# Kernel tuning notes

Measured on AMD Instinct MI355X. Metric: run time of the kernel, lower is better.

Reference implementation:

```python
import jax, jax.numpy as jnp
import numpy as np

D, IN_CH, H, W = 4, 13, 384, 384
EMBED, HID, N_COLORS = 64, 32, 11


def conv(x, w, b, stride=1, pad=0):
    y = jax.lax.conv_general_dilated(
        x, w, window_strides=(stride, stride),
        padding=[(pad, pad), (pad, pad)],
        dimension_numbers=('NCHW', 'OIHW', 'NCHW'))
    return y + b[None, :, None, None]


def setup_inputs() -> dict:
    key = jax.random.key(0)
    ks = jax.random.split(key, 16)
    s = 0.05
    return {
        'demo_inputs': jax.random.normal(ks[0], (D, IN_CH, H, W), jnp.float32),
        'demo_outputs': jax.random.normal(ks[1], (D, IN_CH, H, W), jnp.float32),
        'test_input': jax.random.normal(ks[2], (IN_CH, H, W), jnp.float32),
        'enc_w1': jax.random.normal(ks[3], (32, 26, 3, 3), jnp.float32) * s,
        'enc_b1': jnp.zeros((32,), jnp.float32),
        'enc_w2': jax.random.normal(ks[4], (64, 32, 3, 3), jnp.float32) * s,
        'enc_b2': jnp.zeros((64,), jnp.float32),
        'enc_w3': jax.random.normal(ks[5], (64, 64, 3, 3), jnp.float32) * s,
        'enc_b3': jnp.zeros((64,), jnp.float32),
        'enc_lw': jax.random.normal(ks[6], (EMBED, 64), jnp.float32) * s,
        'enc_lb': jnp.zeros((EMBED,), jnp.float32),
        'stem_w': jax.random.normal(ks[7], (HID, IN_CH, 3, 3), jnp.float32) * s,
        'stem_b': jnp.zeros((HID,), jnp.float32),
        'upd_w1': jax.random.normal(ks[8], (HID, HID + EMBED, 3, 3), jnp.float32) * s,
        'upd_b1': jnp.zeros((HID,), jnp.float32),
        'upd_w2': jax.random.normal(ks[9], (HID, HID, 1, 1), jnp.float32) * s,
        'upd_b2': jnp.zeros((HID,), jnp.float32),
        'tau_w': jax.random.normal(ks[10], (HID, HID + EMBED, 1, 1), jnp.float32) * s,
        'tau_b': jnp.zeros((HID,), jnp.float32),
        'dec_w': jax.random.normal(ks[11], (N_COLORS, HID, 1, 1), jnp.float32) * s,
        'dec_b': jnp.zeros((N_COLORS,), jnp.float32),
        'n_steps': 8,
    }


def reference(demo_inputs, demo_outputs, test_input,
              enc_w1, enc_b1, enc_w2, enc_b2, enc_w3, enc_b3, enc_lw, enc_lb,
              stem_w, stem_b, upd_w1, upd_b1, upd_w2, upd_b2,
              tau_w, tau_b, dec_w, dec_b, n_steps):
    # encode_demos: concat each (in, out) pair along channels -> [D, 2*in_ch, H, W]
    pairs = jnp.concatenate([demo_inputs, demo_outputs], axis=1)
    h = jax.nn.relu(conv(pairs, enc_w1, enc_b1, stride=1, pad=1))
    h = jax.nn.relu(conv(h, enc_w2, enc_b2, stride=2, pad=1))
    h = jax.nn.relu(conv(h, enc_w3, enc_b3, stride=2, pad=1))
    h = h.mean(axis=(2, 3))                      # AdaptiveAvgPool2d(1) + Flatten -> [D, 64]
    emb = h @ enc_lw.T + enc_lb                  # [D, embed_dim]
    task_embed = emb.mean(axis=0)                # [embed_dim]

    x = test_input[None]                         # [1, in_ch, H, W]
    Hh, Ww = x.shape[2], x.shape[3]
    te = jnp.broadcast_to(task_embed[None, :, None, None], (1, task_embed.shape[0], Hh, Ww))
    state = jax.nn.relu(conv(x, stem_w, stem_b, stride=1, pad=1))
    for _ in range(n_steps):
        ctx = jnp.concatenate([state, te], axis=1)   # [1, hid+embed, H, W]
        delta = conv(jax.nn.relu(conv(ctx, upd_w1, upd_b1, stride=1, pad=1)),
                     upd_w2, upd_b2, stride=1, pad=0)
        beta = jax.nn.sigmoid(conv(ctx, tau_w, tau_b, stride=1, pad=0))
        state = beta * state + (1.0 - beta) * delta
    return conv(state, dec_w, dec_b, stride=1, pad=0)  # [1, N_COLORS, H, W]
```

## Files before the change

kernel.cpp:

```cpp
#include <hip/hip_runtime.h>

#define HW 147456

typedef __attribute__((ext_vector_type(8))) short bf16x8;
typedef __attribute__((ext_vector_type(4))) float f32x4;

__device__ __forceinline__ float bf2f(unsigned short u) {
    return __uint_as_float(((unsigned)u) << 16);
}
__device__ __forceinline__ unsigned short f2bf(float f) {
    unsigned u = __float_as_uint(f);
    return (unsigned short)((u + 0x7fffu + ((u >> 16) & 1u)) >> 16);
}

struct TJobs {
    const float* src[5];
    float* dst[5];
    int cout[5], cintot[5], k[5], coutp[5];
    int start[6];
};

__global__ __launch_bounds__(256) void transpose_all_k(TJobs J) {
    int gid = blockIdx.x * 256 + threadIdx.x;
    if (gid >= J.start[5]) return;
    int j = 0;
#pragma unroll
    for (int t = 1; t < 5; ++t)
        if (gid >= J.start[t]) j = t;
    int li = gid - J.start[j];
    int coutp = J.coutp[j], K = J.k[j];
    int co = li % coutp;
    int kk = (li / coutp) % K;
    int cin = li / (coutp * K);
    J.dst[j][li] = (co < J.cout[j]) ? J.src[j][((co * J.cintot[j]) + cin) * K + kk] : 0.f;
}

struct WJobs {
    const float* src[4];
    unsigned short* dst[4];
    int cout[4], cin[4], cintot[4], cinp[4];
    int start[5];
};

__global__ __launch_bounds__(256) void transpose_wbf_k(WJobs J) {
    int gid = blockIdx.x * 256 + threadIdx.x;
    if (gid >= J.start[4]) return;
    int j = 0;
#pragma unroll
    for (int t = 1; t < 4; ++t)
        if (gid >= J.start[t]) j = t;
    int li = gid - J.start[j];
    int cinp = J.cinp[j];
    int ci = li % cinp;
    int co = (li / cinp) % J.cout[j];
    int tap = li / (cinp * J.cout[j]);
    float v = (ci < J.cin[j]) ? J.src[j][((co * J.cintot[j]) + ci) * 9 + tap] : 0.f;
    J.dst[j][li] = f2bf(v);
}

template <int CIN, int CP, int COUT, int S, int OX, int OY, int MW, bool RELU>
__global__ __launch_bounds__(256, MW) void mfma_conv_k(
    const float* __restrict__ in0, const float* __restrict__ in1, int split,
    long off0base, long off1base, long zs0, long zs1, int inW, int inH,
    const unsigned short* __restrict__ wB,
    const float* __restrict__ bias,
    float* __restrict__ out, long outZS) {
    constexpr int XT = (OX - 1) * S + 3;
    constexpr int YT = (OY - 1) * S + 3;
    constexpr int CINK = (CIN + 31) & ~31;
    constexpr int KST = CINK / 32;
    constexpr int NCG = COUT / 16;
    constexpr int NTX = OX / 16;
    constexpr int NSP = NTX * OY;
    constexpr int NTASK = NSP * NCG;
    constexpr int NT4 = NTASK / 4;
    constexpr int NSLOT = YT * XT;
    static_assert(NTASK % 4 == 0, "tasks per wave");
    static_assert(NSP % NT4 == 0, "wave must own a single cout-group");
    static_assert(CP % 8 == 0 && CP >= CINK, "LDS cin pad");
    static_assert((CP / 8) % 2 == 1, "odd chunk stride for bank spread");
    __shared__ __align__(16) unsigned short tile[NSLOT * CP];
    const int tid = threadIdx.x;
    const int bx = blockIdx.x, by = blockIdx.y, z = blockIdx.z;
    const long o0 = off0base + (long)z * zs0;
    const long o1 = off1base + (long)z * zs1;
    const int outW = inW / S, outH = inH / S;
    const int gx0 = bx * OX * S - 1;
    const int gy0 = by * OY * S - 1;

#pragma unroll 1
    for (int s = tid; s < NSLOT; s += 256) {
        const int sy = s / XT;
        const int lx = s - sy * XT;
        const int gy = gy0 + sy;
        const int gx = gx0 + lx;
        const bool ok = ((unsigned)gy < (unsigned)inH) && ((unsigned)gx < (unsigned)inW);
        const long pix = (long)gy * inW + gx;
#pragma unroll
        for (int h = 0; h < CINK / 8; ++h) {
            bf16x8 v;
#pragma unroll
            for (int e = 0; e < 8; ++e) {
                const int c = h * 8 + e;
                float f = 0.f;
                if (c < CIN && ok) {
                    const float* base = (c < split)
                        ? in0 + o0 + (long)c * inH * inW
                        : in1 + o1 + (long)(c - split) * inH * inW;
                    f = base[pix];
                }
                v[e] = (short)f2bf(f);
            }
            *(bf16x8*)(tile + s * CP + h * 8) = v;
        }
    }
    __syncthreads();

    const int wv = tid >> 6;
    const int l = tid & 63;
    const int ln = l & 15;
    const int lk = l >> 4;
    const int cg = (wv * NT4) / NSP;
    bf16x8 bfr[9 * KST];
#pragma unroll
    for (int tap = 0; tap < 9; ++tap)
#pragma unroll
        for (int h = 0; h < KST; ++h)
            bfr[tap * KST + h] = *(const bf16x8*)(wB + ((long)(tap * COUT + cg * 16 + ln)) * CINK + h * 32 + lk * 8);
    const float bv = bias[cg * 16 + ln];
#pragma unroll 1
    for (int t = 0; t < NT4; ++t) {
        const int sp = wv * NT4 + t - cg * NSP;
        const int tx = sp % NTX;
        const int ty = sp / NTX;
        f32x4 acc;
        acc[0] = bv; acc[1] = bv; acc[2] = bv; acc[3] = bv;
#pragma unroll
        for (int ky = 0; ky < 3; ++ky) {
#pragma unroll
            for (int kx = 0; kx < 3; ++kx) {
                const int yb = ty * S + ky;
                const int xb = (tx * 16 + ln) * S + kx;
                const unsigned short* ap = tile + (yb * XT + xb) * CP + lk * 8;
#pragma unroll
                for (int h = 0; h < KST; ++h) {
                    bf16x8 a = *(const bf16x8*)(ap + h * 32);
                    acc = __builtin_amdgcn_mfma_f32_16x16x32_bf16(a, bfr[(ky * 3 + kx) * KST + h], acc, 0, 0, 0);
                }
            }
        }
        const int ox = bx * OX + tx * 16 + lk * 4;
        const int oy = by * OY + ty;
        float4 o;
        if constexpr (RELU) {
            o.x = fmaxf(acc[0], 0.f);
            o.y = fmaxf(acc[1], 0.f);
            o.z = fmaxf(acc[2], 0.f);
            o.w = fmaxf(acc[3], 0.f);
        } else {
            o.x = acc[0]; o.y = acc[1]; o.z = acc[2]; o.w = acc[3];
        }
        *(float4*)(out + (long)z * outZS + ((long)(cg * 16 + ln) * outH + oy) * outW + ox) = o;
    }
}

template <int CIN, int CCHUNK, int WCH, int COUT, int STRIDE, int TW, int CO_PER, int MW>
__global__ __launch_bounds__(256, MW) void conv3x3_k(
    const float* __restrict__ in0, const float* __restrict__ in1, int split,
    long inOff0, long inOff1, long zs0, long zs1, int inW, int inH,
    const float* __restrict__ wT, const float* __restrict__ bias,
    float* __restrict__ out, long outZS) {
    constexpr int NCG = COUT / CO_PER;
    constexpr int NPXG = 256 / NCG;
    constexpr int NXG = TW / 4;
    constexpr int TH = NPXG / NXG;
    constexpr int INW = (TW - 1) * STRIDE + 3;
    constexpr int INH = (TH - 1) * STRIDE + 3;
    constexpr int WIN = 3 * STRIDE + 3;
    constexpr int XV = (INW + 6) / 4;
    constexpr int LDSW = XV * 4 + 1;
    constexpr int SLOTS = INH * XV;
    static_assert(NPXG % NXG == 0 && NPXG * NCG == 256, "thread mapping");
    static_assert(CIN % CCHUNK == 0 && CCHUNK % WCH == 0, "chunking");
    static_assert(SLOTS <= 256, "staging slots");
    __shared__ float tile[CCHUNK][INH][LDSW];
    __shared__ __align__(16) float wlds[WCH * 9 * COUT];
    const int tid = threadIdx.x;
    const int cg = tid / NPXG;
    const int pg = tid % NPXG;
    const int xg = pg % NXG;
    const int yy = pg / NXG;
    const int bx = blockIdx.x, by = blockIdx.y, z = blockIdx.z;
    const int outW = inW / STRIDE, outH = inH / STRIDE;
    const long off0 = inOff0 + (long)z * zs0;
    const long off1 = inOff1 + (long)z * zs1;
    float* outp = out + (long)z * outZS;
    const bool sact = tid < SLOTS;
    const int sr = tid / XV;
    const int sx = tid - sr * XV;
    const int gxs = bx * TW * STRIDE - 4 + sx * 4;
    const int gy0 = by * TH * STRIDE - 1;

    float acc[4][CO_PER];
    {
        float bv[CO_PER];
#pragma unroll
        for (int jj = 0; jj < CO_PER; jj += 4) {
            float4 b4 = *(const float4*)(bias + cg * CO_PER + jj);
            bv[jj] = b4.x; bv[jj + 1] = b4.y; bv[jj + 2] = b4.z; bv[jj + 3] = b4.w;
        }
#pragma unroll
        for (int p = 0; p < 4; ++p)
#pragma unroll
            for (int j = 0; j < CO_PER; ++j) acc[p][j] = bv[j];
    }

    for (int ch = 0; ch < CIN; ch += CCHUNK) {
        if (sact) {
            const int gy = gy0 + sr;
            const bool yok = (unsigned)gy < (unsigned)inH;
            const bool xfull = (gxs >= 0) && (gxs + 3 < inW);
#pragma unroll
            for (int c = 0; c < CCHUNK; ++c) {
                const int gc = ch + c;
                const float* row = (gc < split)
                    ? in0 + off0 + ((long)gc * inH + gy) * inW
                    : in1 + off1 + ((long)(gc - split) * inH + gy) * inW;
                float4 v = {0.f, 0.f, 0.f, 0.f};
                if (yok) {
                    if (xfull) {
                        v = *(const float4*)(row + gxs);
                    } else {
                        float t[4];
#pragma unroll
                        for (int k = 0; k < 4; ++k) {
                            int gx = gxs + k;
                            t[k] = ((unsigned)gx < (unsigned)inW) ? row[gx] : 0.f;
                        }
                        v = {t[0], t[1], t[2], t[3]};
                    }
                }
                float* dst = &tile[c][sr][sx * 4];
                dst[0] = v.x; dst[1] = v.y; dst[2] = v.z; dst[3] = v.w;
            }
        }
#pragma unroll 1
        for (int wc = 0; wc < CCHUNK; wc += WCH) {
            {
                const float4* wsrc = (const float4*)(wT + (long)(ch + wc) * 9 * COUT);
                float4* wdst = (float4*)wlds;
                constexpr int CNT = WCH * 9 * COUT / 4;
                for (int i = tid; i < CNT; i += 256) wdst[i] = wsrc[i];
            }
            __syncthreads();
#pragma unroll 1
            for (int c = 0; c < WCH; ++c) {
#pragma unroll
                for (int ky = 0; ky < 3; ++ky) {
                    const int ty = yy * STRIDE + ky;
                    const int tx0 = xg * 4 * STRIDE + 3;
                    float xw[WIN];
#pragma unroll
                    for (int i = 0; i < WIN; ++i) xw[i] = tile[wc + c][ty][tx0 + i];
#pragma unroll
                    for (int dx = 0; dx < 3; ++dx) {
                        const float* wp = wlds + ((c * 3 + ky) * 3 + dx) * COUT + cg * CO_PER;
                        float wv[CO_PER];
#pragma unroll
                        for (int jj = 0; jj < CO_PER; jj += 4) {
                            float4 w4 = *(const float4*)(wp + jj);
                            wv[jj] = w4.x; wv[jj + 1] = w4.y; wv[jj + 2] = w4.z; wv[jj + 3] = w4.w;
                        }
#pragma unroll
                        for (int p = 0; p < 4; ++p) {
                            float xv = xw[p * STRIDE + dx];
#pragma unroll
                            for (int j = 0; j < CO_PER; ++j) acc[p][j] = fmaf(xv, wv[j], acc[p][j]);
                        }
                    }
                }
            }
            __syncthreads();
        }
    }

    const int ox0 = bx * TW + xg * 4;
    const int oy = by * TH + yy;
#pragma unroll
    for (int j = 0; j < CO_PER; ++j) {
        int co = cg * CO_PER + j;
        float4 o;
        o.x = fmaxf(acc[0][j], 0.f);
        o.y = fmaxf(acc[1][j], 0.f);
        o.z = fmaxf(acc[2][j], 0.f);
        o.w = fmaxf(acc[3][j], 0.f);
        *(float4*)(outp + ((long)co * outH + oy) * outW + ox0) = o;
    }
}

__global__ __launch_bounds__(256) void pool_k(const float* __restrict__ enc3base,
                                              long zstride,
                                              float* __restrict__ meanout) {
    int z = blockIdx.x >> 6;
    int c = blockIdx.x & 63;
    const float* p = enc3base + (long)z * zstride + (long)c * 9216;
    float s = 0.f;
    for (int i = threadIdx.x; i < 9216; i += 256) s += p[i];
    __shared__ float red[256];
    red[threadIdx.x] = s;
    __syncthreads();
    for (int o = 128; o > 0; o >>= 1) {
        if (threadIdx.x < o) red[threadIdx.x] += red[threadIdx.x + o];
        __syncthreads();
    }
    if (threadIdx.x == 0) meanout[z * 64 + c] = red[0] * (1.f / 9216.f);
}

__global__ __launch_bounds__(256) void prep_te_k(
    const float* __restrict__ means, const float* __restrict__ lw,
    const float* __restrict__ lb, const float* __restrict__ tauw,
    const float* __restrict__ taub, const float* __restrict__ w1,
    const float* __restrict__ b1,
    float* __restrict__ tauc, float* __restrict__ wsum,
    float* __restrict__ bias2) {
    __shared__ float tes[64];
    int t = threadIdx.x;
    if (t < 64) {
        float s = 0.f;
        for (int d = 0; d < 4; ++d)
            for (int c = 0; c < 64; ++c) s += means[d * 64 + c] * lw[t * 64 + c];
        tes[t] = lb[t] + 0.25f * s;
    }
    __syncthreads();
    if (t < 32) {
        float s = taub[t];
        for (int e = 0; e < 64; ++e) s += tauw[t * 96 + 32 + e] * tes[e];
        tauc[t] = s;
    }
    for (int i = t; i < 288; i += 256) {
        int co = i % 32;
        int k = i / 32;
        float s = 0.f;
        for (int e = 0; e < 64; ++e) s += w1[((co * 96) + 32 + e) * 9 + k] * tes[e];
        wsum[i] = s;
    }
    __syncthreads();
    if (t < 32) {
        float s = b1[t];
        for (int k = 0; k < 9; ++k) s += wsum[k * 32 + t];
        bias2[t] = s;
    }
}

__global__ __launch_bounds__(256, 2) void nca_step_fused_k(
    const float* __restrict__ sold, float* __restrict__ snew,
    const unsigned short* __restrict__ wBE,
    const float* __restrict__ bias2,
    const float* __restrict__ wsum,
    const float* __restrict__ w2T, const float* __restrict__ b2,
    const float* __restrict__ tauT, const float* __restrict__ tauc) {
    __shared__ __align__(16) unsigned short tile[204 * 40];
    __shared__ __align__(16) float ss[32][132];
    __shared__ __align__(16) float sw2[1024], stu[1024];
    __shared__ float sb2[32], stc[32];
    const int tid = threadIdx.x;
    const int bx = blockIdx.x, by = blockIdx.y;
    const int gx0 = bx * 32 - 1;
    const int gy0 = by * 4 - 1;

    for (int i = tid; i < 1024; i += 256) {
        sw2[i] = w2T[i];
        stu[i] = tauT[i];
    }
    if (tid < 32) {
        sb2[tid] = b2[tid];
        stc[tid] = tauc[tid];
    }
    if (tid < 204) {
        const int sy = tid / 34;
        const int lx = tid - sy * 34;
        const int gy = gy0 + sy;
        const int gx = gx0 + lx;
        const bool ok = ((unsigned)gy < 384u) && ((unsigned)gx < 384u);
        const long pix = (long)gy * 384 + gx;
        const bool ctr = (sy >= 1) && (sy <= 4) && (lx >= 1) && (lx <= 32);
        const int pxl = (sy - 1) * 32 + (lx - 1);
#pragma unroll
        for (int h = 0; h < 4; ++h) {
            bf16x8 v;
#pragma unroll
            for (int e = 0; e < 8; ++e) {
                const int c = h * 8 + e;
                float f = ok ? sold[(long)c * HW + pix] : 0.f;
                v[e] = (short)f2bf(f);
                if (ctr) ss[c][pxl] = f;
            }
            *(bf16x8*)(tile + tid * 40 + h * 8) = v;
        }
    }
    __syncthreads();

    const int wv = tid >> 6;
    const int l = tid & 63;
    const int ln = l & 15;
    const int lk = l >> 4;
    const int cg = wv >> 1;
    const int co = cg * 16 + ln;
    bf16x8 bfr[9];
#pragma unroll
    for (int tap = 0; tap < 9; ++tap)
        bfr[tap] = *(const bf16x8*)(wBE + ((long)(tap * 32 + co)) * 32 + lk * 8);
    const float bv = bias2[co];
    f32x4 accs[4];
#pragma unroll
    for (int t = 0; t < 4; ++t) {
        const int sp = (wv & 1) * 4 + t;
        const int tx = sp & 1;
        const int ty = sp >> 1;
        f32x4 acc;
        acc[0] = bv; acc[1] = bv; acc[2] = bv; acc[3] = bv;
#pragma unroll
        for (int ky = 0; ky < 3; ++ky) {
#pragma unroll
            for (int kx = 0; kx < 3; ++kx) {
                const unsigned short* ap = tile + ((ty + ky) * 34 + tx * 16 + ln + kx) * 40 + lk * 8;
                bf16x8 a = *(const bf16x8*)ap;
                acc = __builtin_amdgcn_mfma_f32_16x16x32_bf16(a, bfr[ky * 3 + kx], acc, 0, 0, 0);
            }
        }
        accs[t] = acc;
    }
    __syncthreads();

    unsigned short (*h1s)[136] = (unsigned short(*)[136])tile;
#pragma unroll
    for (int t = 0; t < 4; ++t) {
        const int sp = (wv & 1) * 4 + t;
        const int tx = sp & 1;
        const int ty = sp >> 1;
        const int gy = by * 4 + ty;
        const int gxb = bx * 32 + tx * 16 + lk * 4;
        float hv[4] = {accs[t][0], accs[t][1], accs[t][2], accs[t][3]};
        const bool ytop = (gy == 0), ybot = (gy == 383);
#pragma unroll
        for (int r = 0; r < 4; ++r) {
            const int gx = gxb + r;
            const bool xl = (gx == 0), xr = (gx == 383);
            if (xl | xr | ytop | ybot) {
                float h = hv[r];
#pragma unroll
                for (int ky = 0; ky < 3; ++ky)
#pragma unroll
                    for (int kx = 0; kx < 3; ++kx) {
                        bool inval = (ky == 0 && ytop) || (ky == 2 && ybot) ||
                                     (kx == 0 && xl) || (kx == 2 && xr);
                        if (inval) h -= wsum[(ky * 3 + kx) * 32 + co];
                    }
                hv[r] = h;
            }
        }
        ushort4 ho;
        ho.x = f2bf(fmaxf(hv[0], 0.f));
        ho.y = f2bf(fmaxf(hv[1], 0.f));
        ho.z = f2bf(fmaxf(hv[2], 0.f));
        ho.w = f2bf(fmaxf(hv[3], 0.f));
        *(ushort4*)(&h1s[co][ty * 32 + tx * 16 + lk * 4]) = ho;
    }
    __syncthreads();

    const int cg2 = tid >> 5;
    const int pg = tid & 31;
    const int p0 = pg * 4;
    float accd[4][4], acct[4][4];
    {
        float dv[4], tv[4];
#pragma unroll
        for (int j = 0; j < 4; ++j) {
            dv[j] = sb2[cg2 * 4 + j];
            tv[j] = stc[cg2 * 4 + j];
        }
#pragma unroll
        for (int p = 0; p < 4; ++p)
#pragma unroll
            for (int j = 0; j < 4; ++j) { accd[p][j] = dv[j]; acct[p][j] = tv[j]; }
    }
#pragma unroll 2
    for (int ci = 0; ci < 32; ++ci) {
        float hv[4], sv[4];
#pragma unroll
        for (int p = 0; p < 4; ++p) {
            hv[p] = bf2f(h1s[ci][p0 + p]);
            sv[p] = ss[ci][p0 + p];
        }
        float4 wd4 = *(const float4*)(sw2 + ci * 32 + cg2 * 4);
        float4 wt4 = *(const float4*)(stu + ci * 32 + cg2 * 4);
        float wdv[4] = {wd4.x, wd4.y, wd4.z, wd4.w};
        float wtv[4] = {wt4.x, wt4.y, wt4.z, wt4.w};
#pragma unroll
        for (int p = 0; p < 4; ++p) {
#pragma unroll
            for (int j = 0; j < 4; ++j) {
                accd[p][j] = fmaf(hv[p], wdv[j], accd[p][j]);
                acct[p][j] = fmaf(sv[p], wtv[j], acct[p][j]);
            }
        }
    }
    const int yl = p0 >> 5;
    const int xl2 = p0 & 31;
    const long obase = ((long)(by * 4 + yl)) * 384 + bx * 32 + xl2;
#pragma unroll
    for (int j = 0; j < 4; ++j) {
        const int co2 = cg2 * 4 + j;
        float ov[4];
#pragma unroll
        for (int p = 0; p < 4; ++p) {
            float sown = ss[co2][p0 + p];
            float beta = 1.f / (1.f + __expf(-acct[p][j]));
            ov[p] = beta * sown + (1.f - beta) * accd[p][j];
        }
        float4 o = {ov[0], ov[1], ov[2], ov[3]};
        *(float4*)(snew + (long)co2 * HW + obase) = o;
    }
}

__global__ __launch_bounds__(256) void dec_k(const float* __restrict__ st,
                                             const float* __restrict__ dT,
                                             const float* __restrict__ db,
                                             float* __restrict__ out) {
    int gid = blockIdx.x * 256 + threadIdx.x;
    long px0 = (long)gid * 2;
    float acc[11][2];
#pragma unroll
    for (int co = 0; co < 11; ++co) {
        float b = db[co];
        acc[co][0] = b;
        acc[co][1] = b;
    }
    for (int ci = 0; ci < 32; ++ci) {
        float2 s2 = *(const float2*)(st + (long)ci * HW + px0);
        const float* wp = dT + ci * 12;
        float4 w0 = *(const float4*)wp, w1 = *(const float4*)(wp + 4), w2 = *(const float4*)(wp + 8);
        float wv[12] = {w0.x, w0.y, w0.z, w0.w, w1.x, w1.y, w1.z, w1.w, w2.x, w2.y, w2.z, w2.w};
#pragma unroll
        for (int co = 0; co < 11; ++co) {
            acc[co][0] = fmaf(s2.x, wv[co], acc[co][0]);
            acc[co][1] = fmaf(s2.y, wv[co], acc[co][1]);
        }
    }
#pragma unroll
    for (int co = 0; co < 11; ++co) {
        float2 o = {acc[co][0], acc[co][1]};
        *(float2*)(out + (long)co * HW + px0) = o;
    }
}

extern "C" void kernel_launch(void* const* d_in, const int* in_sizes, int n_in,
                              void* d_out, int out_size, void* d_ws, size_t ws_size,
                              hipStream_t stream) {
    float* out = (float*)d_out;
    const float* demo_in = (const float*)d_in[0];
    const float* demo_out = (const float*)d_in[1];
    const float* test_in = (const float*)d_in[2];
    const float* enc_w1 = (const float*)d_in[3];
    const float* enc_b1 = (const float*)d_in[4];
    const float* enc_w2 = (const float*)d_in[5];
    const float* enc_b2 = (const float*)d_in[6];
    const float* enc_w3 = (const float*)d_in[7];
    const float* enc_b3 = (const float*)d_in[8];
    const float* enc_lw = (const float*)d_in[9];
    const float* enc_lb = (const float*)d_in[10];
    const float* stem_w = (const float*)d_in[11];
    const float* stem_b = (const float*)d_in[12];
    const float* upd_w1 = (const float*)d_in[13];
    const float* upd_b1 = (const float*)d_in[14];
    const float* upd_w2 = (const float*)d_in[15];
    const float* upd_b2 = (const float*)d_in[16];
    const float* tau_w = (const float*)d_in[17];
    const float* tau_b = (const float*)d_in[18];
    const float* dec_w = (const float*)d_in[19];
    const float* dec_b = (const float*)d_in[20];

    float* Wb = (float*)d_ws;
    float* wT_D = Wb + 0;
    float* w2T  = Wb + 3744;
    float* tauT = Wb + 4768;
    float* decT = Wb + 5792;
    float* tauc = Wb + 6176;
    float* wsum = Wb + 6208;
    float* means = Wb + 6496;
    float* bias2 = Wb + 6752;
    unsigned short* wB1 = (unsigned short*)(Wb + 6784);
    unsigned short* wB2 = (unsigned short*)(Wb + 11392);
    unsigned short* wB3 = (unsigned short*)(Wb + 20608);
    unsigned short* wBE = (unsigned short*)(Wb + 39040);
    float* big = Wb + 45056;

    const long PD = 7667712;
    const long E1 = 4718592, E2 = 2359296;
    size_t wsf = ws_size / 4;
    int NZ = 1;
    if (wsf >= 45056 + 4 * (size_t)PD) NZ = 4;
    else if (wsf >= 45056 + 2 * (size_t)PD) NZ = 2;

    TJobs J;
    {
        const float* srcs[5] = {stem_w, upd_w2, tau_w, dec_w, dec_w};
        float* dsts[5] = {wT_D, w2T, tauT, decT, decT};
        int couts[5] = {32, 32, 32, 11, 0};
        int cintots[5] = {13, 32, 96, 32, 32};
        int ks[5] = {9, 1, 1, 1, 1};
        int cinsels[5] = {13, 32, 32, 32, 0};
        int coutps[5] = {32, 32, 32, 12, 12};
        int acc0 = 0;
        for (int j = 0; j < 5; ++j) {
            J.src[j] = srcs[j]; J.dst[j] = dsts[j];
            J.cout[j] = couts[j]; J.cintot[j] = cintots[j];
            J.k[j] = ks[j]; J.coutp[j] = coutps[j];
            J.start[j] = acc0;
            acc0 += cinsels[j] * ks[j] * coutps[j];
        }
        J.start[5] = acc0;
        transpose_all_k<<<(acc0 + 255) / 256, 256, 0, stream>>>(J);
    }
    WJobs W;
    {
        const float* srcs[4] = {enc_w1, enc_w2, enc_w3, upd_w1};
        unsigned short* dsts[4] = {wB1, wB2, wB3, wBE};
        int couts[4] = {32, 64, 64, 32};
        int cins[4] = {26, 32, 64, 32};
        int cintots[4] = {26, 32, 64, 96};
        int cinps[4] = {32, 32, 64, 32};
        int acc0 = 0;
        for (int j = 0; j < 4; ++j) {
            W.src[j] = srcs[j]; W.dst[j] = dsts[j];
            W.cout[j] = couts[j]; W.cin[j] = cins[j];
            W.cintot[j] = cintots[j]; W.cinp[j] = cinps[j];
            W.start[j] = acc0;
            acc0 += 9 * couts[j] * cinps[j];
        }
        W.start[4] = acc0;
        transpose_wbf_k<<<(acc0 + 255) / 256, 256, 0, stream>>>(W);
    }

    for (int d0 = 0; d0 < 4; d0 += NZ) {
        mfma_conv_k<26, 40, 32, 1, 64, 4, 5, true><<<dim3(6, 96, NZ), 256, 0, stream>>>(
            demo_in, demo_out, 13, (long)d0 * 13 * HW, (long)d0 * 13 * HW,
            13L * HW, 13L * HW, 384, 384, wB1, enc_b1, big, PD);
        mfma_conv_k<32, 40, 64, 2, 32, 2, 5, true><<<dim3(6, 96, NZ), 256, 0, stream>>>(
            big, big, 32, 0, 0, PD, PD, 384, 384, wB2, enc_b2, big + E1, PD);
        mfma_conv_k<64, 72, 64, 2, 16, 2, 5, true><<<dim3(6, 48, NZ), 256, 0, stream>>>(
            big + E1, big + E1, 64, 0, 0, PD, PD, 192, 192, wB3, enc_b3,
            big + E1 + E2, PD);
        pool_k<<<64 * NZ, 256, 0, stream>>>(big + E1 + E2, PD, means + d0 * 64);
    }
    prep_te_k<<<1, 256, 0, stream>>>(means, enc_lw, enc_lb, tau_w, tau_b, upd_w1,
                                     upd_b1, tauc, wsum, bias2);

    float* sA = big;
    float* sX = big + E1;
    conv3x3_k<13, 13, 13, 32, 1, 32, 8, 5><<<dim3(12, 48, 1), 256, 0, stream>>>(
        test_in, test_in, 13, 0, 0, 0, 0, 384, 384, wT_D, stem_b, sA, 0);

    float* a = sA;
    float* b = sX;
    for (int s = 0; s < 8; ++s) {
        nca_step_fused_k<<<dim3(12, 96), 256, 0, stream>>>(
            a, b, wBE, bias2, wsum, w2T, upd_b2, tauT, tauc);
        float* t = a; a = b; b = t;
    }
    dec_k<<<288, 256, 0, stream>>>(a, decT, dec_b, out);
}
```

Measured before the change: 490.3 us.

## Store encoder intermediates in bf16 and fuse decoder into final NCA step

Encoder conv1 and conv2 now write their activations as bf16 rather than fp32, and the following convs read bf16 directly. This halves intermediate traffic, and those kernels already converted to bf16 when filling shared memory, so precision should be unchanged. The separate 1x1 decoder kernel is removed. The last NCA step applies the decoder from shared memory and skips writing the final state to global memory. The workspace layout changes, and NZ is forced to at least 2 with no fallback to 1.

```diff
diff --git a/kernel.cpp b/kernel.cpp
--- a/kernel.cpp
+++ b/kernel.cpp
@@ -58,13 +58,14 @@
     J.dst[j][li] = f2bf(v);
 }
 
-template <int CIN, int CP, int COUT, int S, int OX, int OY, int MW, bool RELU>
+template <int CIN, int CP, int COUT, int S, int OX, int OY, int MW, bool RELU,
+          bool INBF, bool OUTBF>
 __global__ __launch_bounds__(256, MW) void mfma_conv_k(
-    const float* __restrict__ in0, const float* __restrict__ in1, int split,
+    const void* __restrict__ vin0, const void* __restrict__ vin1, int split,
     long off0base, long off1base, long zs0, long zs1, int inW, int inH,
     const unsigned short* __restrict__ wB,
     const float* __restrict__ bias,
-    float* __restrict__ out, long outZS) {
+    void* __restrict__ vout, long outZS) {
     constexpr int XT = (OX - 1) * S + 3;
     constexpr int YT = (OY - 1) * S + 3;
     constexpr int CINK = (CIN + 31) & ~31;
@@ -102,14 +103,18 @@
 #pragma unroll
             for (int e = 0; e < 8; ++e) {
                 const int c = h * 8 + e;
-                float f = 0.f;
+                unsigned short raw = 0;
                 if (c < CIN && ok) {
-                    const float* base = (c < split)
-                        ? in0 + o0 + (long)c * inH * inW
-                        : in1 + o1 + (long)(c - split) * inH * inW;
-                    f = base[pix];
+                    const long ofs = (c < split)
+                        ? o0 + (long)c * inH * inW + pix
+                        : o1 + (long)(c - split) * inH * inW + pix;
+                    const void* src = (c < split) ? vin0 : vin1;
+                    if constexpr (INBF)
+                        raw = ((const unsigned short*)src)[ofs];
+                    else
+                        raw = f2bf(((const float*)src)[ofs]);
                 }
-                v[e] = (short)f2bf(f);
+                v[e] = (short)raw;
             }
             *(bf16x8*)(tile + s * CP + h * 8) = v;
         }
@@ -151,16 +156,18 @@
         }
         const int ox = bx * OX + tx * 16 + lk * 4;
         const int oy = by * OY + ty;
-        float4 o;
-        if constexpr (RELU) {
-            o.x = fmaxf(acc[0], 0.f);
-            o.y = fmaxf(acc[1], 0.f);
-            o.z = fmaxf(acc[2], 0.f);
-            o.w = fmaxf(acc[3], 0.f);
+        float r[4];
+#pragma unroll
+        for (int e = 0; e < 4; ++e) r[e] = RELU ? fmaxf(acc[e], 0.f) : acc[e];
+        const long oidx = (long)z * outZS + ((long)(cg * 16 + ln) * outH + oy) * outW + ox;
+        if constexpr (OUTBF) {
+            ushort4 o;
+            o.x = f2bf(r[0]); o.y = f2bf(r[1]); o.z = f2bf(r[2]); o.w = f2bf(r[3]);
+            *(ushort4*)((unsigned short*)vout + oidx) = o;
         } else {
-            o.x = acc[0]; o.y = acc[1]; o.z = acc[2]; o.w = acc[3];
-        }
-        *(float4*)(out + (long)z * outZS + ((long)(cg * 16 + ln) * outH + oy) * outW + ox) = o;
+            float4 o = {r[0], r[1], r[2], r[3]};
+            *(float4*)((float*)vout + oidx) = o;
+        }
     }
 }
 
@@ -352,17 +359,21 @@
     }
 }
 
+template <bool LAST>
 __global__ __launch_bounds__(256, 2) void nca_step_fused_k(
     const float* __restrict__ sold, float* __restrict__ snew,
     const unsigned short* __restrict__ wBE,
     const float* __restrict__ bias2,
     const float* __restrict__ wsum,
     const float* __restrict__ w2T, const float* __restrict__ b2,
-    const float* __restrict__ tauT, const float* __restrict__ tauc) {
+    const float* __restrict__ tauT, const float* __restrict__ tauc,
+    const float* __restrict__ decT, const float* __restrict__ db,
+    float* __restrict__ dout) {
     __shared__ __align__(16) unsigned short tile[204 * 40];
     __shared__ __align__(16) float ss[32][132];
     __shared__ __align__(16) float sw2[1024], stu[1024];
     __shared__ float sb2[32], stc[32];
+    __shared__ float sdec[384], sdb[12];
     const int tid = threadIdx.x;
     const int bx = blockIdx.x, by = blockIdx.y;
     const int gx0 = bx * 32 - 1;
@@ -375,6 +386,10 @@
     if (tid < 32) {
         sb2[tid] = b2[tid];
         stc[tid] = tauc[tid];
+    }
+    if constexpr (LAST) {
+        for (int i = tid; i < 384; i += 256) sdec[i] = decT[i];
+        if (tid < 11) sdb[tid] = db[tid];
     }
     if (tid < 204) {
         const int sy = tid / 34;
@@ -505,52 +520,52 @@
             }
         }
     }
-    const int yl = p0 >> 5;
-    const int xl2 = p0 & 31;
-    const long obase = ((long)(by * 4 + yl)) * 384 + bx * 32 + xl2;
+    float ov4[4][4];
 #pragma unroll
     for (int j = 0; j < 4; ++j) {
-        const int co2 = cg2 * 4 + j;
-        float ov[4];
 #pragma unroll
         for (int p = 0; p < 4; ++p) {
-            float sown = ss[co2][p0 + p];
+            float sown = ss[cg2 * 4 + j][p0 + p];
             float beta = 1.f / (1.f + __expf(-acct[p][j]));
-            ov[p] = beta * sown + (1.f - beta) * accd[p][j];
-        }
-        float4 o = {ov[0], ov[1], ov[2], ov[3]};
-        *(float4*)(snew + (long)co2 * HW + obase) = o;
-    }
-}
-
-__global__ __launch_bounds__(256) void dec_k(const float* __restrict__ st,
-                                             const float* __restrict__ dT,
-                                             const float* __restrict__ db,
-                                             float* __restrict__ out) {
-    int gid = blockIdx.x * 256 + threadIdx.x;
-    long px0 = (long)gid * 2;
-    float acc[11][2];
-#pragma unroll
-    for (int co = 0; co < 11; ++co) {
-        float b = db[co];
-        acc[co][0] = b;
-        acc[co][1] = b;
-    }
-    for (int ci = 0; ci < 32; ++ci) {
-        float2 s2 = *(const float2*)(st + (long)ci * HW + px0);
-        const float* wp = dT + ci * 12;
-        float4 w0 = *(const float4*)wp, w1 = *(const float4*)(wp + 4), w2 = *(const float4*)(wp + 8);
-        float wv[12] = {w0.x, w0.y, w0.z, w0.w, w1.x, w1.y, w1.z, w1.w, w2.x, w2.y, w2.z, w2.w};
-#pragma unroll
-        for (int co = 0; co < 11; ++co) {
-            acc[co][0] = fmaf(s2.x, wv[co], acc[co][0]);
-            acc[co][1] = fmaf(s2.y, wv[co], acc[co][1]);
-        }
-    }
-#pragma unroll
-    for (int co = 0; co < 11; ++co) {
-        float2 o = {acc[co][0], acc[co][1]};
-        *(float2*)(out + (long)co * HW + px0) = o;
+            ov4[j][p] = beta * sown + (1.f - beta) * accd[p][j];
+        }
+    }
+    if constexpr (!LAST) {
+        const int yl = p0 >> 5;
+        const int xl2 = p0 & 31;
+        const long obase = ((long)(by * 4 + yl)) * 384 + bx * 32 + xl2;
+#pragma unroll
+        for (int j = 0; j < 4; ++j) {
+            float4 o = {ov4[j][0], ov4[j][1], ov4[j][2], ov4[j][3]};
+            *(float4*)(snew + (long)(cg2 * 4 + j) * HW + obase) = o;
+        }
+    } else {
+        __syncthreads();
+#pragma unroll
+        for (int j = 0; j < 4; ++j)
+#pragma unroll
+            for (int p = 0; p < 4; ++p)
+                ss[cg2 * 4 + j][p0 + p] = ov4[j][p];
+        __syncthreads();
+        const int q = tid & 127;
+        const int half = tid >> 7;
+        const int nco = half ? 5 : 6;
+        float acc[6];
+#pragma unroll
+        for (int j = 0; j < 6; ++j) acc[j] = (j < nco) ? sdb[half * 6 + j] : 0.f;
+#pragma unroll 4
+        for (int ci = 0; ci < 32; ++ci) {
+            float sv = ss[ci][q];
+            const float* wp = sdec + ci * 12 + half * 6;
+#pragma unroll
+            for (int j = 0; j < 6; ++j) acc[j] = fmaf(sv, wp[j], acc[j]);
+        }
+        const int yq = q >> 5;
+        const long pxg = ((long)(by * 4 + yq)) * 384 + bx * 32 + (q & 31);
+#pragma unroll
+        for (int j = 0; j < 6; ++j) {
+            if (j < nco) dout[(long)(half * 6 + j) * HW + pxg] = acc[j];
+        }
     }
 }
 
@@ -595,12 +610,14 @@
     unsigned short* wBE = (unsigned short*)(Wb + 39040);
     float* big = Wb + 45056;
 
-    const long PD = 7667712;
-    const long E1 = 4718592, E2 = 2359296;
+    const long E1 = 4718592;
+    const long E2 = 2359296;
+    const long E3 = 589824;
     size_t wsf = ws_size / 4;
-    int NZ = 1;
-    if (wsf >= 45056 + 4 * (size_t)PD) NZ = 4;
-    else if (wsf >= 45056 + 2 * (size_t)PD) NZ = 2;
+    int NZ = (wsf >= (size_t)(45056 + 4 * 4128768L)) ? 4 : 2;
+    unsigned short* enc1b = (unsigned short*)big;
+    unsigned short* enc2b = enc1b + (long)NZ * E1;
+    float* enc3f = (float*)(enc2b + (long)NZ * E2);
 
     TJobs J;
     {
@@ -643,15 +660,21 @@
     }
 
     for (int d0 = 0; d0 < 4; d0 += NZ) {
-        mfma_conv_k<26, 40, 32, 1, 64, 4, 5, true><<<dim3(6, 96, NZ), 256, 0, stream>>>(
+        mfma_conv_k<26, 40, 32, 1, 64, 4, 5, true, false, true>
+            <<<dim3(6, 96, NZ), 256, 0, stream>>>(
             demo_in, demo_out, 13, (long)d0 * 13 * HW, (long)d0 * 13 * HW,
-            13L * HW, 13L * HW, 384, 384, wB1, enc_b1, big, PD);
-        mfma_conv_k<32, 40, 64, 2, 32, 2, 5, true><<<dim3(6, 96, NZ), 256, 0, stream>>>(
-            big, big, 32, 0, 0, PD, PD, 384, 384, wB2, enc_b2, big + E1, PD);
-        mfma_conv_k<64, 72, 64, 2, 16, 2, 5, true><<<dim3(6, 48, NZ), 256, 0, stream>>>(
-            big + E1, big + E1, 64, 0, 0, PD, PD, 192, 192, wB3, enc_b3,
-            big + E1 + E2, PD);
-        pool_k<<<64 * NZ, 256, 0, stream>>>(big + E1 + E2, PD, means + d0 * 64);
+            13L * HW, 13L * HW, 384, 384, wB1, enc_b1,
+            enc1b + (long)d0 * E1, E1);
+        mfma_conv_k<32, 40, 64, 2, 32, 2, 5, true, true, true>
+            <<<dim3(6, 96, NZ), 256, 0, stream>>>(
+            enc1b + (long)d0 * E1, enc1b + (long)d0 * E1, 32, 0, 0, E1, E1,
+            384, 384, wB2, enc_b2, enc2b + (long)d0 * E2, E2);
+        mfma_conv_k<64, 72, 64, 2, 16, 2, 5, true, true, false>
+            <<<dim3(6, 48, NZ), 256, 0, stream>>>(
+            enc2b + (long)d0 * E2, enc2b + (long)d0 * E2, 64, 0, 0, E2, E2,
+            192, 192, wB3, enc_b3, enc3f + (long)d0 * E3, E3);
+        pool_k<<<64 * NZ, 256, 0, stream>>>(enc3f + (long)d0 * E3, E3,
+                                            means + d0 * 64);
     }
     prep_te_k<<<1, 256, 0, stream>>>(means, enc_lw, enc_lb, tau_w, tau_b, upd_w1,
                                      upd_b1, tauc, wsum, bias2);
@@ -663,10 +686,11 @@
 
     float* a = sA;
     float* b = sX;
-    for (int s = 0; s < 8; ++s) {
-        nca_step_fused_k<<<dim3(12, 96), 256, 0, stream>>>(
-            a, b, wBE, bias2, wsum, w2T, upd_b2, tauT, tauc);
+    for (int s = 0; s < 7; ++s) {
+        nca_step_fused_k<false><<<dim3(12, 96), 256, 0, stream>>>(
+            a, b, wBE, bias2, wsum, w2T, upd_b2, tauT, tauc, decT, dec_b, out);
         float* t = a; a = b; b = t;
     }
-    dec_k<<<288, 256, 0, stream>>>(a, decT, dec_b, out);
-}
+    nca_step_fused_k<true><<<dim3(12, 96), 256, 0, stream>>>(
+        a, b, wBE, bias2, wsum, w2T, upd_b2, tauT, tauc, decT, dec_b, out);
+}
```

After: 481.3 us. Within noise of the previous version (-1.8%).
